# Kernel tuning notes

Hardware: AMD Instinct MI355X
Metric: run time of the kernel (lower is better)

The kernel has to match this reference:

```python
import jax, jax.numpy as jnp
import numpy as np

B, S, D, H, NS = 4, 4096, 1024, 16, 128
DA, DF = 512, 4096
DK, DV = DA // H, D // H  # 32, 64
TEMP = 1.0
EPS = 1e-6


def setup_inputs() -> dict:
    key = jax.random.key(0)
    ks = jax.random.split(key, 8)
    r = lambda k, shp: jax.random.normal(k, shp, jnp.float32) * 0.02
    return dict(
        x=jax.random.normal(ks[0], (B, S, D), jnp.float32),
        mask=jnp.ones((B, S), jnp.float32),
        residual_scale=jnp.ones((1,), jnp.float32),
        w_q=r(ks[1], (D, DA)), b_q=jnp.zeros((DA,), jnp.float32),
        w_kv=r(ks[2], (D, DA + D)), b_kv=jnp.zeros((DA + D,), jnp.float32),
        w_s=r(ks[3], (D, H * NS)), b_s=jnp.zeros((H * NS,), jnp.float32),
        w_cat=r(ks[4], (D, D)), b_cat=jnp.zeros((D,), jnp.float32),
        norm1_w=jnp.ones((D,), jnp.float32), norm2_w=jnp.ones((D,), jnp.float32),
        w1=r(ks[5], (D, DF)), b1=jnp.zeros((DF,), jnp.float32),
        w2=r(ks[6], (DF, D)), b2=jnp.zeros((D,), jnp.float32),
    )


def _rms(x, w):
    return x * jax.lax.rsqrt(jnp.mean(x * x, axis=-1, keepdims=True) + EPS) * w


def _forward(x, mask, residual_scale, w_q, b_q, w_kv, b_kv, w_s, b_s,
             w_cat, b_cat, norm1_w, norm2_w, w1, b1, w2, b2):
    neg = jnp.finfo(jnp.float32).min
    xn = _rms(x, norm1_w)
    q = (xn @ w_q + b_q).reshape(B, S, H, DK).transpose(0, 2, 1, 3)        # [B,H,S,DK]
    kv = (xn @ w_kv + b_kv).reshape(B, S, H, DK + DV).transpose(0, 2, 1, 3)  # [B,H,S,DK+DV]
    k_raw, v_raw = kv[..., :DK], kv[..., DK:]

    # DSZRC sampler: per-head soft routing of S tokens -> NS sampled KV rows
    logits = (x @ w_s + b_s).reshape(B, S, H, NS).transpose(0, 2, 3, 1)    # [B,H,NS,S]
    logits = jnp.where(mask[:, None, None, :] > 0, logits, neg)
    probs = jax.nn.softmax(logits / TEMP, axis=-1)
    kv_s = jnp.einsum('bhms,bhsd->bhmd', probs, kv)                        # [B,H,NS,DK+DV]
    k_s, v_s = kv_s[..., :DK], kv_s[..., DK:]

    # branch 1: dense SDPA over sampled KV
    scale = 1.0 / np.sqrt(DK).astype(np.float32)
    att = jax.nn.softmax(jnp.einsum('bhqd,bhkd->bhqk', q, k_s) * scale, axis=-1)
    out1 = jnp.einsum('bhqk,bhkd->bhqd', att, v_s)                         # [B,H,S,DV]

    # branch 2: fp16 sliding-window flash attn, left window = NS (keys i-NS..i)
    f16 = lambda t: t.astype(jnp.float16).astype(jnp.float32)
    qh, kh, vh = f16(q), f16(k_raw), f16(v_raw)
    bs = NS
    nb = S // bs
    qb = qh.reshape(B, H, nb, bs, DK)
    kb = kh.reshape(B, H, nb, bs, DK)
    vb = vh.reshape(B, H, nb, bs, DV)
    shift = lambda t: jnp.concatenate([jnp.zeros_like(t[:, :, :1]), t[:, :, :-1]], axis=2)
    kctx = jnp.concatenate([shift(kb), kb], axis=3)                        # [B,H,nb,2bs,DK]
    vctx = jnp.concatenate([shift(vb), vb], axis=3)
    sc = jnp.einsum('bhnad,bhnkd->bhnak', qb, kctx) * scale                # [B,H,nb,bs,2bs]
    a = jnp.arange(bs)[:, None]
    bcol = jnp.arange(2 * bs)[None, :]
    band = (bcol >= a) & (bcol <= a + NS)                                  # 0 <= q-k <= NS
    tpos = jnp.arange(nb)[:, None, None]
    valid = band[None] & ((tpos > 0) | (bcol >= bs)[None])                 # no keys before pos 0
    p = jax.nn.softmax(jnp.where(valid[None, None], sc, neg), axis=-1)
    out2 = f16(jnp.einsum('bhnak,bhnkd->bhnad', p, vctx)).reshape(B, H, S, DV)

    x_att = (out1 + out2).transpose(0, 2, 1, 3).reshape(B, S, D)
    x = x + (x_att @ w_cat + b_cat) * residual_scale
    h = _rms(x, norm2_w)
    x = x + (jax.nn.gelu(h @ w1 + b1, approximate=False) @ w2 + b2) * residual_scale
    return x


def reference(x, mask, residual_scale, w_q, b_q, w_kv, b_kv, w_s, b_s,
              w_cat, b_cat, norm1_w, norm2_w, w1, b1, w2, b2):
    return _forward(x, mask, residual_scale, w_q, b_q, w_kv, b_kv, w_s, b_s,
                    w_cat, b_cat, norm1_w, norm2_w, w1, b1, w2, b2)
```

## Files before the change

kernel.cpp:

```cpp
#include <hip/hip_runtime.h>
#include <cstdint>
#include <cmath>

#define DEV __device__ __forceinline__

using f16 = _Float16;
typedef f16  f16x4 __attribute__((ext_vector_type(4)));
typedef f16  f16x8 __attribute__((ext_vector_type(8)));
typedef float f32x4 __attribute__((ext_vector_type(4)));

constexpr int Bq = 4, Sq = 4096, Hq = 16;
constexpr int Tq = Bq * Sq;

DEV void gload_lds16(const void* g, void* l) {
  __builtin_amdgcn_global_load_lds(
      (const __attribute__((address_space(1))) void*)g,
      (__attribute__((address_space(3))) void*)l, 16, 0, 0);
}

DEV void stage_swz(const char* gbase, long gstride, char* lds, int nbytes,
                   int rowlog, int swzmask) {
  int tid = threadIdx.x;
  for (int b0 = 0; b0 < nbytes; b0 += 4096) {
    int P = b0 + tid * 16;
    int L = P ^ (((P >> rowlog) & swzmask) << 4);
    long row  = L >> rowlog;
    int  colb = L & ((1 << rowlog) - 1);
    gload_lds16(gbase + row * gstride + colb, lds + b0 + (tid & ~63) * 16);
  }
}

DEV void stage_swz512(const char* gbase, long gstride, char* lds, int nbytes,
                      int rowlog, int swzmask) {
  int tid = threadIdx.x;
  for (int b0 = 0; b0 < nbytes; b0 += 8192) {
    int P = b0 + tid * 16;
    int L = P ^ (((P >> rowlog) & swzmask) << 4);
    long row  = L >> rowlog;
    int  colb = L & ((1 << rowlog) - 1);
    gload_lds16(gbase + row * gstride + colb, lds + b0 + (tid & ~63) * 16);
  }
}

DEV void pipe_barrier() {
  __builtin_amdgcn_sched_barrier(0);
  __builtin_amdgcn_s_barrier();
  asm volatile("" ::: "memory");
  __builtin_amdgcn_sched_barrier(0);
}

DEV float wave16_max(float v) {
#pragma unroll
  for (int d = 1; d < 16; d <<= 1) v = fmaxf(v, __shfl_xor(v, d, 64));
  return v;
}
DEV float wave16_sum(float v) {
#pragma unroll
  for (int d = 1; d < 16; d <<= 1) v += __shfl_xor(v, d, 64);
  return v;
}

__global__ __launch_bounds__(256) void wcast_k(const float* __restrict__ W,
                                               f16* __restrict__ Wt, int K, int N) {
  int n0 = blockIdx.x * 32, k0 = blockIdx.y * 32;
  __shared__ float tile[32][33];
  int tid = threadIdx.x, r = tid >> 5, c = tid & 31;
#pragma unroll
  for (int i = 0; i < 4; ++i)
    tile[r + i * 8][c] = W[(size_t)(k0 + r + i * 8) * N + n0 + c];
  __syncthreads();
#pragma unroll
  for (int i = 0; i < 4; ++i) {
    int rr = r + i * 8;
    Wt[(size_t)(n0 + rr) * K + k0 + c] = (f16)tile[c][rr];
  }
}

__global__ void bias_concat_k(const float* __restrict__ bq, const float* __restrict__ bkv,
                              float* __restrict__ out) {
  int i = blockIdx.x * 256 + threadIdx.x;
  out[i] = (i < 512) ? bq[i] : bkv[i - 512];
}

__global__ __launch_bounds__(256) void rmsnorm_k(const float* __restrict__ x,
                                                 const float* __restrict__ w,
                                                 f16* __restrict__ xn) {
  int row = blockIdx.x, tid = threadIdx.x;
  float4 v = ((const float4*)(x + (size_t)row * 1024))[tid];
  float ss = v.x * v.x + v.y * v.y + v.z * v.z + v.w * v.w;
#pragma unroll
  for (int d = 1; d < 64; d <<= 1) ss += __shfl_xor(ss, d, 64);
  __shared__ float red[4];
  if ((tid & 63) == 0) red[tid >> 6] = ss;
  __syncthreads();
  float tot = red[0] + red[1] + red[2] + red[3];
  float r = rsqrtf(tot * (1.0f / 1024.0f) + 1e-6f);
  float4 wv = ((const float4*)w)[tid];
  f16x4 o;
  o[0] = (f16)(v.x * r * wv.x); o[1] = (f16)(v.y * r * wv.y);
  o[2] = (f16)(v.z * r * wv.z); o[3] = (f16)(v.w * r * wv.w);
  *(f16x4*)(xn + (size_t)row * 1024 + tid * 4) = o;
}

template <int MODE>
__global__ __launch_bounds__(256) void gemm_k(const f16* __restrict__ A, const f16* __restrict__ Bt,
                                              const float* __restrict__ bias,
                                              float* __restrict__ outF,
                                              const float* __restrict__ resid,
                                              const float* __restrict__ rsp,
                                              int M, int N, int K, int lda, int ldb) {
  __shared__ alignas(16) char smA[2][16384];
  __shared__ alignas(16) char smB[2][16384];
  int nwgx = gridDim.x, nbc = gridDim.y;
  int bidl = blockIdx.y * nwgx + blockIdx.x;
  int cpx = (nwgx * nbc) >> 3;
  int xcd = bidl & 7, pos = bidl >> 3;
  int rpm = cpx / nbc;
  int nbi = pos / rpm, mbi = pos % rpm;
  int mb = xcd * rpm + mbi;
  long n0 = (long)nbi * 128;
  int tid = threadIdx.x, lane = tid & 63, wv = tid >> 6, wr = wv >> 1, wc = wv & 1;
  long m0 = (long)mb * 128;
  f32x4 acc[4][4] = {};
  const char* Ab = (MODE == 7) ? nullptr : (const char*)(A + m0 * lda);
  const char* Bb = (const char*)(Bt + n0 * ldb);

  auto stageAB = [&](int buf, int k0) {
    stage_swz(Bb + (long)k0 * 2, (long)ldb * 2, smB[buf], 16384, 7, 7);
    if (MODE == 7) {
      const char* Ab7 = (const char*)(A + (((m0 >> 12) * 16 + (k0 >> 6)) * 4096 + (m0 & 4095)) * 64);
      stage_swz(Ab7, 128, smA[buf], 16384, 7, 7);
    } else {
      stage_swz(Ab + (long)k0 * 2, (long)lda * 2, smA[buf], 16384, 7, 7);
    }
  };
  auto doCompute = [&](const char* cA, const char* cB) {
#pragma unroll
    for (int kk = 0; kk < 2; ++kk) {
      int kbyte = kk * 64 + (lane >> 4) * 16;
      f16x8 aF[4], bF[4];
#pragma unroll
      for (int m = 0; m < 4; ++m) {
        int L = (wr * 64 + m * 16 + (lane & 15)) * 128 + kbyte;
        aF[m] = *(const f16x8*)(cA + (L ^ (((L >> 7) & 7) << 4)));
      }
#pragma unroll
      for (int n = 0; n < 4; ++n) {
        int L = (wc * 64 + n * 16 + (lane & 15)) * 128 + kbyte;
        bF[n] = *(const f16x8*)(cB + (L ^ (((L >> 7) & 7) << 4)));
      }
#pragma unroll
      for (int m = 0; m < 4; ++m)
#pragma unroll
        for (int n = 0; n < 4; ++n)
          acc[m][n] = __builtin_amdgcn_mfma_f32_16x16x32_f16(aF[m], bF[n], acc[m][n], 0, 0, 0);
    }
  };

  int T = K >> 6;
  stageAB(0, 0);
  stageAB(1, 64);
  asm volatile("s_waitcnt vmcnt(8)" ::: "memory");
  pipe_barrier();
  for (int t = 0; t < T; ++t) {
    doCompute(smA[t & 1], smB[t & 1]);
    pipe_barrier();
    if (t + 2 < T) {
      stageAB(t & 1, (t + 2) << 6);
      asm volatile("s_waitcnt vmcnt(8)" ::: "memory");
    } else {
      asm volatile("s_waitcnt vmcnt(0)" ::: "memory");
    }
    if (t + 1 < T) pipe_barrier();
  }
  float rsv = rsp[0];
#pragma unroll
  for (int m = 0; m < 4; ++m)
#pragma unroll
    for (int n = 0; n < 4; ++n) {
      long gn = n0 + wc * 64 + n * 16 + (lane & 15);
      float bv = bias[gn];
      long rbase = m0 + wr * 64 + m * 16 + (lane >> 4) * 4;
#pragma unroll
      for (int i = 0; i < 4; ++i) {
        long gm = rbase + i;
        float v = acc[m][n][i] + bv;
        long idx = gm * N + gn;
        outF[idx] = resid[idx] + v * rsv;
      }
    }
}

template <int MODE>
__global__ __launch_bounds__(512) void gemm256_k(const f16* __restrict__ A, const f16* __restrict__ Bt,
                                                 const float* __restrict__ bias,
                                                 f16* __restrict__ o1, f16* __restrict__ o2,
                                                 f16* __restrict__ o3,
                                                 const float* __restrict__ resid,
                                                 int M, int N, int K, int lda, int ldb, int pp) {
  __shared__ alignas(16) char smA[2][32768];
  __shared__ alignas(16) char smB[2][32768];
  int nwgx = gridDim.x, nbc = gridDim.y;
  int bidl = blockIdx.y * nwgx + blockIdx.x;
  int cpx = (nwgx * nbc) >> 3;
  int xcd = bidl & 7, pos = bidl >> 3;
  int rpm = cpx / nbc;
  int nbi = pos / rpm, mbi = pos % rpm;
  int mb = xcd * rpm + mbi;
  long n0 = (long)nbi * 256;
  int tid = threadIdx.x, lane = tid & 63, wv = tid >> 6;
  int wr = wv >> 2, wc = wv & 3;
  long m0;
  long t0 = 0;
  int bq = 0;
  if (MODE == 5) {
    bq = mb >> 3; int sb = mb & 7;
    m0 = (long)sb * 256;
    t0 = (long)bq * 4096 + (long)pp * 2048 + m0;
  } else {
    m0 = (long)mb * 256;
  }
  f32x4 acc[8][4] = {};
  const char* Ab = (MODE == 5) ? nullptr : (const char*)(A + m0 * lda);
  const char* Bb = (const char*)(Bt + n0 * ldb);

  auto stageAB = [&](int buf, int k0) {
    stage_swz512(Bb + (long)k0 * 2, (long)ldb * 2, smB[buf], 32768, 7, 7);
    if (MODE == 5) {
      int P = tid * 16;
#pragma unroll
      for (int b0 = 0; b0 < 32768; b0 += 8192) {
        int PP = b0 + P;
        int L = PP ^ (((PP >> 7) & 7) << 4);
        int row = L >> 7, colf = (L & 127) >> 1;
        const float* src = resid + (size_t)(t0 + row) * 1024 + k0 + colf;
        float4 u0 = *(const float4*)src;
        float4 u1 = *(const float4*)(src + 4);
        f16x8 o;
        o[0] = (f16)u0.x; o[1] = (f16)u0.y; o[2] = (f16)u0.z; o[3] = (f16)u0.w;
        o[4] = (f16)u1.x; o[5] = (f16)u1.y; o[6] = (f16)u1.z; o[7] = (f16)u1.w;
        *(f16x8*)(smA[buf] + PP) = o;
      }
    } else {
      stage_swz512(Ab + (long)k0 * 2, (long)lda * 2, smA[buf], 32768, 7, 7);
    }
  };
  auto doCompute = [&](const char* cA, const char* cB) {
#pragma unroll
    for (int kk = 0; kk < 2; ++kk) {
      int kbyte = kk * 64 + (lane >> 4) * 16;
      f16x8 aF[8], bF[4];
#pragma unroll
      for (int m = 0; m < 8; ++m) {
        int L = (wr * 128 + m * 16 + (lane & 15)) * 128 + kbyte;
        aF[m] = *(const f16x8*)(cA + (L ^ (((L >> 7) & 7) << 4)));
      }
#pragma unroll
      for (int n = 0; n < 4; ++n) {
        int L = (wc * 64 + n * 16 + (lane & 15)) * 128 + kbyte;
        bF[n] = *(const f16x8*)(cB + (L ^ (((L >> 7) & 7) << 4)));
      }
#pragma unroll
      for (int m = 0; m < 8; ++m)
#pragma unroll
        for (int n = 0; n < 4; ++n)
          acc[m][n] = __builtin_amdgcn_mfma_f32_16x16x32_f16(aF[m], bF[n], acc[m][n], 0, 0, 0);
    }
  };

  if constexpr (MODE == 5) {
    stageAB(0, 0);
    __syncthreads();
    int cur = 0;
    for (int k0 = 0; k0 < K; k0 += 64) {
      if (k0 + 64 < K) stageAB(cur ^ 1, k0 + 64);
      doCompute(smA[cur], smB[cur]);
      __syncthreads();
      cur ^= 1;
    }
  } else {
    int T = K >> 6;
    stageAB(0, 0);
    stageAB(1, 64);
    asm volatile("s_waitcnt vmcnt(8)" ::: "memory");
    pipe_barrier();
    for (int t = 0; t < T; ++t) {
      doCompute(smA[t & 1], smB[t & 1]);
      pipe_barrier();
      if (t + 2 < T) {
        stageAB(t & 1, (t + 2) << 6);
        asm volatile("s_waitcnt vmcnt(8)" ::: "memory");
      } else {
        asm volatile("s_waitcnt vmcnt(0)" ::: "memory");
      }
      if (t + 1 < T) pipe_barrier();
    }
  }
#pragma unroll
  for (int m = 0; m < 8; ++m)
#pragma unroll
    for (int n = 0; n < 4; ++n) {
      long gn = n0 + wc * 64 + n * 16 + (lane & 15);
      float bv = bias[gn];
      long rbase = m0 + wr * 128 + m * 16 + (lane >> 4) * 4;
      if (MODE == 4) {
        long b = rbase >> 12, s = rbase & 4095;
        if (gn < 512) {
          long h = gn >> 5, dk = gn & 31;
#pragma unroll
          for (int i = 0; i < 4; ++i)
            o1[(((size_t)b * 16 + h) * 4096 + s + i) * 32 + dk] = (f16)(acc[m][n][i] + bv);
        } else {
          long c2 = gn - 512, h = c2 / 96, j = c2 % 96;
          if (j < 32) {
#pragma unroll
            for (int i = 0; i < 4; ++i)
              o2[(((size_t)b * 16 + h) * 4096 + s + i) * 32 + j] = (f16)(acc[m][n][i] + bv);
          } else {
            f16x4 pk;
#pragma unroll
            for (int i = 0; i < 4; ++i) pk[i] = (f16)(acc[m][n][i] + bv);
            *(f16x4*)(o3 + (((size_t)b * 16 + h) * 64 + (j - 32)) * 4096 + s) = pk;
          }
        }
      } else {
#pragma unroll
        for (int i = 0; i < 4; ++i) {
          long gm = rbase + i;
          float v = acc[m][n][i] + bv;
          if (MODE == 3) {
            float u = v * 0.7978845608028654f * (1.f + 0.044715f * v * v);
            float e = __expf(fminf(2.f * u, 80.f));
            o1[gm * N + gn] = (f16)(v * (e / (e + 1.f)));
          } else {
            o1[((size_t)bq * 2048 + gn) * 2048 + gm] = (f16)v;
          }
        }
      }
    }
}

__global__ __launch_bounds__(256) void kvs_k(const f16* __restrict__ lt,
                                             const f16* __restrict__ kh,
                                             const f16* __restrict__ vT,
                                             const float* __restrict__ mask,
                                             float* __restrict__ pacc, int pass) {
  int gx = blockIdx.x, nsb = gx & 3, sc = gx >> 2;
  int h = blockIdx.y, b = blockIdx.z;
  int bh = b * 16 + h;
  __shared__ alignas(16) char smA[4096];
  __shared__ alignas(16) f16 smB[112][88];
  int tid = threadIdx.x, lane = tid & 63, w = tid >> 6;
  int mf = w >> 1, nb0 = (w & 1) * 4, nfr = (w & 1) ? 3 : 4;
  for (int idx = tid; idx < 16 * 64; idx += 256) {
    int r = 96 + (idx >> 6), c2 = idx & 63;
    smB[r][c2] = (r == 96) ? (f16)1.0f : (f16)0.0f;
  }
  f32x4 acc[4] = {};
  const f16* ltb = lt + ((size_t)bh * 128 + nsb * 32) * 2048;
  for (int it = 0; it < 4; ++it) {
    int sl0 = sc * 256 + it * 64;
    int s0g = pass * 2048 + sl0;
    __syncthreads();
    {
      int P = tid * 16;
      int L = P ^ (((P >> 7) & 7) << 4);
      int row = L >> 7, colf = (L & 127) >> 1;
      f16x8 lv = *(const f16x8*)(ltb + (size_t)row * 2048 + sl0 + colf);
      const float* mrow = mask + (size_t)b * 4096 + s0g + colf;
      float4 m0v = *(const float4*)mrow, m1v = *(const float4*)(mrow + 4);
      float mm[8] = {m0v.x, m0v.y, m0v.z, m0v.w, m1v.x, m1v.y, m1v.z, m1v.w};
      f16x8 o;
#pragma unroll
      for (int j = 0; j < 8; ++j)
        o[j] = (f16)((mm[j] > 0.f) ? expf((float)lv[j] - 8.0f) : 0.0f);
      *(f16x8*)(smA + P) = o;
    }
    {
      int sl = tid >> 2, jg = (tid & 3) * 8;
      f16x8 u = *(const f16x8*)(kh + ((size_t)bh * 4096 + s0g + sl) * 32 + jg);
#pragma unroll
      for (int j = 0; j < 8; ++j) smB[jg + j][sl] = u[j];
    }
#pragma unroll
    for (int half = 0; half < 2; ++half) {
      int task = tid + half * 256;
      int dv = task >> 3, sl0v = (task & 7) * 8;
      f16x8 u = *(const f16x8*)(vT + ((size_t)bh * 64 + dv) * 4096 + s0g + sl0v);
      *(f16x8*)(&smB[32 + dv][sl0v]) = u;
    }
    __syncthreads();
#pragma unroll
    for (int kk = 0; kk < 2; ++kk) {
      int kbyte = kk * 64 + (lane >> 4) * 16;
      int L = (mf * 16 + (lane & 15)) * 128 + kbyte;
      f16x8 aF = *(const f16x8*)(smA + (L ^ (((L >> 7) & 7) << 4)));
#pragma unroll
      for (int n = 0; n < 4; ++n)
        if (n < nfr) {
          f16x8 bF = *(const f16x8*)((const char*)smB + ((nb0 + n) * 16 + (lane & 15)) * 176 + kbyte);
          acc[n] = __builtin_amdgcn_mfma_f32_16x16x32_f16(aF, bF, acc[n], 0, 0, 0);
        }
    }
  }
  int slot = pass * 8 + sc;
  float* pb = pacc + (((size_t)bh * 4 + nsb) * 16 + slot) * 3584;
#pragma unroll
  for (int n = 0; n < 4; ++n)
    if (n < nfr) {
      int col = (nb0 + n) * 16 + (lane & 15);
#pragma unroll
      for (int i = 0; i < 4; ++i) {
        int nsrow = mf * 16 + (lane >> 4) * 4 + i;
        pb[(size_t)nsrow * 112 + col] = acc[n][i];
      }
    }
}

__global__ __launch_bounds__(256) void kvs_fin_k(const float* __restrict__ pacc,
                                                 f16* __restrict__ ks, f16* __restrict__ vst) {
  int bh = blockIdx.x, tid = threadIdx.x;
  __shared__ float den[128];
  const float* base = pacc + (size_t)bh * 4 * 16 * 3584;
  if (tid < 128) {
    int nsb = tid >> 5, nsl = tid & 31;
    float d = 0.f;
#pragma unroll
    for (int slot = 0; slot < 16; ++slot)
      d += base[((size_t)nsb * 16 + slot) * 3584 + (size_t)nsl * 112 + 96];
    den[tid] = d;
  }
  __syncthreads();
  for (int e = tid; e < 12288; e += 256) {
    int ns = e / 96, j = e % 96;
    int nsb = ns >> 5, nsl = ns & 31;
    float sv = 0.f;
#pragma unroll
    for (int slot = 0; slot < 16; ++slot)
      sv += base[((size_t)nsb * 16 + slot) * 3584 + (size_t)nsl * 112 + j];
    float v = sv / den[ns];
    if (j < 32) ks[((size_t)bh * 128 + ns) * 32 + j] = (f16)v;
    else        vst[((size_t)bh * 64 + (j - 32)) * 128 + ns] = (f16)v;
  }
}

__global__ __launch_bounds__(256) void att_k(const f16* __restrict__ qh,
                                             const f16* __restrict__ kh,
                                             const f16* __restrict__ vTh,
                                             const f16* __restrict__ ksb,
                                             const f16* __restrict__ vstb,
                                             f16* __restrict__ xatt) {
  int ntj = blockIdx.x, h = blockIdx.y, b = blockIdx.z;
  int nt = ((ntj & 7) << 3) | (ntj >> 3);
  int bh = b * 16 + h, s0 = nt * 64;
  __shared__ alignas(16) char smQ[4096];
  __shared__ alignas(16) char smK[4096];
  __shared__ alignas(16) char smV[8192];
  __shared__ alignas(16) f16 smP[4][16][72];
  int tid = threadIdx.x, lane = tid & 63, w = tid >> 6;
  const float scale = 0.17677669529663687f;
  stage_swz((const char*)(qh + ((size_t)bh * 4096 + s0) * 32), 64, smQ, 4096, 6, 3);

  float mrun[4], lrun[4], m1[4], l1[4];
#pragma unroll
  for (int i = 0; i < 4; ++i) { mrun[i] = -1e30f; lrun[i] = 0.f; m1[i] = -1e30f; l1[i] = 0.f; }
  f32x4 o2[4] = {}, o1[4] = {};

  for (int c = 0; c < 5; ++c) {
    bool win = (c < 3);
    long kb = (long)s0 + (c - 2) * 64;
    if (win && kb < 0) continue;
    __syncthreads();
    if (win) {
      stage_swz((const char*)(kh + ((size_t)bh * 4096 + kb) * 32), 64, smK, 4096, 6, 3);
      stage_swz((const char*)(vTh + (size_t)bh * 64 * 4096 + kb), 8192, smV, 8192, 7, 7);
    } else {
      int sc = c - 3;
      stage_swz((const char*)(ksb + ((size_t)bh * 128 + sc * 64) * 32), 64, smK, 4096, 6, 3);
      stage_swz((const char*)(vstb + (size_t)bh * 64 * 128 + sc * 64), 256, smV, 8192, 7, 7);
    }
    __syncthreads();
    f32x4 s[4] = {};
    {
      int kbyte = (lane >> 4) * 16;
      int Lq = (w * 16 + (lane & 15)) * 64 + kbyte;
      f16x8 aF = *(const f16x8*)(smQ + (Lq ^ (((Lq >> 6) & 3) << 4)));
#pragma unroll
      for (int n = 0; n < 4; ++n) {
        int Lk = (n * 16 + (lane & 15)) * 64 + kbyte;
        f16x8 bF = *(const f16x8*)(smK + (Lk ^ (((Lk >> 6) & 3) << 4)));
        s[n] = __builtin_amdgcn_mfma_f32_16x16x32_f16(aF, bF, s[n], 0, 0, 0);
      }
    }
    float* mr = win ? mrun : m1;
    float* lr = win ? lrun : l1;
    f32x4* oo = win ? o2 : o1;
#pragma unroll
    for (int i = 0; i < 4; ++i) {
      int a2 = w * 16 + (lane >> 4) * 4 + i;
      float nm = mr[i];
#pragma unroll
      for (int n = 0; n < 4; ++n) {
        int kl = n * 16 + (lane & 15);
        bool valid = !win || (c == 1) || (c == 0 ? (kl >= a2) : (kl <= a2));
        float v = valid ? s[n][i] * scale : -1e30f;
        s[n][i] = v; nm = fmaxf(nm, v);
      }
      nm = wave16_max(nm);
      float alpha = expf(mr[i] - nm);
      float sum = 0.f;
#pragma unroll
      for (int n = 0; n < 4; ++n) { float p = expf(s[n][i] - nm); s[n][i] = p; sum += p; }
      sum = wave16_sum(sum);
      lr[i] = lr[i] * alpha + sum;
      mr[i] = nm;
#pragma unroll
      for (int n = 0; n < 4; ++n) oo[n][i] *= alpha;
    }
#pragma unroll
    for (int n = 0; n < 4; ++n)
#pragma unroll
      for (int i = 0; i < 4; ++i)
        smP[w][(lane >> 4) * 4 + i][n * 16 + (lane & 15)] = (f16)s[n][i];
#pragma unroll
    for (int kk = 0; kk < 2; ++kk) {
      int kb2 = kk * 64 + (lane >> 4) * 16;
      f16x8 aP = *(const f16x8*)((const char*)smP[w] + (lane & 15) * 144 + kb2);
#pragma unroll
      for (int n = 0; n < 4; ++n) {
        int dv = n * 16 + (lane & 15);
        int Lv = dv * 128 + kb2;
        f16x8 bV = *(const f16x8*)(smV + (Lv ^ (((Lv >> 7) & 7) << 4)));
        oo[n] = __builtin_amdgcn_mfma_f32_16x16x32_f16(aP, bV, oo[n], 0, 0, 0);
      }
    }
  }
  f16* xb = xatt + ((size_t)bh * 4096 + s0) * 64;
#pragma unroll
  for (int n = 0; n < 4; ++n)
#pragma unroll
    for (int i = 0; i < 4; ++i) {
      int row = w * 16 + (lane >> 4) * 4 + i, dv = n * 16 + (lane & 15);
      xb[(size_t)row * 64 + dv] = (f16)(o2[n][i] / lrun[i] + o1[n][i] / l1[i]);
    }
}

__global__ void sentinel_k(float* out, size_t n, float val) {
  size_t i = (size_t)blockIdx.x * 256 + threadIdx.x;
  size_t stride = (size_t)gridDim.x * 256;
  for (; i < n; i += stride) out[i] = val;
}

constexpr size_t OFF_WQKV = 0;
constexpr size_t OFF_WSC  = OFF_WQKV + 2048ull * 1024 * 2;
constexpr size_t OFF_WCAT = OFF_WSC  + 2048ull * 1024 * 2;
constexpr size_t OFF_W1   = OFF_WCAT + 1024ull * 1024 * 2;
constexpr size_t OFF_W2   = OFF_W1   + 4096ull * 1024 * 2;
constexpr size_t OFF_BQKV = OFF_W2   + 1024ull * 4096 * 2;
constexpr size_t OFF_ZB   = OFF_BQKV + 8192;
constexpr size_t OFF_Q    = OFF_ZB   + 4096;
constexpr size_t OFF_K    = OFF_Q    + (size_t)Tq * 512 * 2;
constexpr size_t OFF_P1   = OFF_K    + (size_t)Tq * 512 * 2;
constexpr size_t OFF_VT   = OFF_P1   + (size_t)Tq * 1024 * 2;
constexpr size_t OFF_KVA  = OFF_VT   + (size_t)Tq * 1024 * 2;
constexpr size_t OFF_KS   = OFF_KVA  + 64ull * 128 * 112 * 4;
constexpr size_t OFF_VST  = OFF_KS   + 64ull * 128 * 32 * 2;
constexpr size_t WS_NEED  = OFF_VST  + 64ull * 64 * 128 * 2;

extern "C" void kernel_launch(void* const* d_in, const int* in_sizes, int n_in,
                              void* d_out, int out_size, void* d_ws, size_t ws_size,
                              hipStream_t stream) {
  float* xo = (float*)d_out;
  if (ws_size < WS_NEED) {
    float val = -(1000.0f + (float)(ws_size / 1000000ull));
    sentinel_k<<<2048, 256, 0, stream>>>(xo, (size_t)out_size, val);
    return;
  }
  const float* x     = (const float*)d_in[0];
  const float* mask  = (const float*)d_in[1];
  const float* rsp   = (const float*)d_in[2];
  const float* w_q   = (const float*)d_in[3];
  const float* b_q   = (const float*)d_in[4];
  const float* w_kv  = (const float*)d_in[5];
  const float* b_kv  = (const float*)d_in[6];
  const float* w_s   = (const float*)d_in[7];
  const float* b_s   = (const float*)d_in[8];
  const float* w_cat = (const float*)d_in[9];
  const float* b_cat = (const float*)d_in[10];
  const float* n1w   = (const float*)d_in[11];
  const float* n2w   = (const float*)d_in[12];
  const float* w1    = (const float*)d_in[13];
  const float* b1    = (const float*)d_in[14];
  const float* w2    = (const float*)d_in[15];
  const float* b2    = (const float*)d_in[16];
  char* ws = (char*)d_ws;

  f16*   wqkv_t = (f16*)(ws + OFF_WQKV);
  f16*   ws_t   = (f16*)(ws + OFF_WSC);
  f16*   wcat_t = (f16*)(ws + OFF_WCAT);
  f16*   w1_t   = (f16*)(ws + OFF_W1);
  f16*   w2_t   = (f16*)(ws + OFF_W2);
  float* bqkv   = (float*)(ws + OFF_BQKV);
  f16*   q_h    = (f16*)(ws + OFF_Q);
  f16*   k_h    = (f16*)(ws + OFF_K);
  f16*   h_h    = (f16*)(ws + OFF_Q);
  f16*   xn_h   = (f16*)(ws + OFF_P1);
  f16*   lt16   = (f16*)(ws + OFF_P1);
  f16*   xatt_h = (f16*)(ws + OFF_P1);
  f16*   g_h    = (f16*)(ws + OFF_P1);
  f16*   vT_h   = (f16*)(ws + OFF_VT);
  f16*   ks_h   = (f16*)(ws + OFF_KS);
  f16*   vst_h  = (f16*)(ws + OFF_VST);

  wcast_k<<<dim3(16, 32),  256, 0, stream>>>(w_q,   wqkv_t,              1024, 512);
  wcast_k<<<dim3(48, 32),  256, 0, stream>>>(w_kv,  wqkv_t + 512 * 1024, 1024, 1536);
  wcast_k<<<dim3(64, 32),  256, 0, stream>>>(w_s,   ws_t,                1024, 2048);
  wcast_k<<<dim3(32, 32),  256, 0, stream>>>(w_cat, wcat_t,              1024, 1024);
  wcast_k<<<dim3(128, 32), 256, 0, stream>>>(w1,    w1_t,                1024, 4096);
  wcast_k<<<dim3(32, 128), 256, 0, stream>>>(w2,    w2_t,                4096, 1024);
  bias_concat_k<<<8, 256, 0, stream>>>(b_q, b_kv, bqkv);

  rmsnorm_k<<<Tq, 256, 0, stream>>>(x, n1w, xn_h);
  gemm256_k<4><<<dim3(64, 8), 512, 0, stream>>>(xn_h, wqkv_t, bqkv, q_h, k_h, vT_h,
                                                nullptr, Tq, 2048, 1024, 1024, 1024, 0);
  for (int p = 0; p < 2; ++p) {
    gemm256_k<5><<<dim3(32, 8), 512, 0, stream>>>(nullptr, ws_t, b_s, lt16, nullptr, nullptr,
                                                  x, 8192, 2048, 1024, 0, 1024, p);
    kvs_k<<<dim3(32, 16, 4), 256, 0, stream>>>(lt16, k_h, vT_h, mask, xo, p);
  }
  kvs_fin_k<<<64, 256, 0, stream>>>(xo, ks_h, vst_h);
  att_k<<<dim3(64, 16, 4), 256, 0, stream>>>(q_h, k_h, vT_h, ks_h, vst_h, xatt_h);
  gemm_k<7><<<dim3(128, 8), 256, 0, stream>>>(xatt_h, wcat_t, b_cat, xo,
                                              x, rsp, Tq, 1024, 1024, 0, 1024);
  rmsnorm_k<<<Tq, 256, 0, stream>>>(xo, n2w, h_h);
  for (int mc = 0; mc < 2; ++mc) {
    const f16* hA = h_h + (size_t)mc * 8192 * 1024;
    float* xoc = xo + (size_t)mc * 8192 * 1024;
    gemm256_k<3><<<dim3(32, 16), 512, 0, stream>>>(hA, w1_t, b1, g_h, nullptr, nullptr,
                                                   nullptr, 8192, 4096, 1024, 1024, 1024, 0);
    gemm_k<2><<<dim3(64, 8), 256, 0, stream>>>(g_h, w2_t, b2, xoc,
                                               xoc, rsp, 8192, 1024, 4096, 4096, 4096);
  }
}
```

Before: 949.8 us.

## Interleave split LDS staging with per-column MFMA phases in GEMM main loops

Restructures the GEMM main loops so global-to-LDS staging of the next A/B tiles is split into halves and issued between four MFMA phases, one per B column block. A fragments for both k-steps are loaded once per tile. Each MFMA phase is wrapped in raised wave priority and sched barriers. Launch bounds now request two blocks per CU. The goal is to hide memory latency behind compute and raise occupancy, at the cost of more register pressure and finer-grained waitcnt logic that could stall or spill.

```diff
diff --git a/kernel.cpp b/kernel.cpp
--- a/kernel.cpp
+++ b/kernel.cpp
@@ -103,12 +103,12 @@
 }
 
 template <int MODE>
-__global__ __launch_bounds__(256) void gemm_k(const f16* __restrict__ A, const f16* __restrict__ Bt,
-                                              const float* __restrict__ bias,
-                                              float* __restrict__ outF,
-                                              const float* __restrict__ resid,
-                                              const float* __restrict__ rsp,
-                                              int M, int N, int K, int lda, int ldb) {
+__global__ __launch_bounds__(256, 2) void gemm_k(const f16* __restrict__ A, const f16* __restrict__ Bt,
+                                                 const float* __restrict__ bias,
+                                                 float* __restrict__ outF,
+                                                 const float* __restrict__ resid,
+                                                 const float* __restrict__ rsp,
+                                                 int M, int N, int K, int lda, int ldb) {
   __shared__ alignas(16) char smA[2][16384];
   __shared__ alignas(16) char smB[2][16384];
   int nwgx = gridDim.x, nbc = gridDim.y;
@@ -125,53 +125,112 @@
   const char* Ab = (MODE == 7) ? nullptr : (const char*)(A + m0 * lda);
   const char* Bb = (const char*)(Bt + n0 * ldb);
 
-  auto stageAB = [&](int buf, int k0) {
-    stage_swz(Bb + (long)k0 * 2, (long)ldb * 2, smB[buf], 16384, 7, 7);
+  auto gstage = [&](const char* gbase, long gstride, char* lds, int half) {
+#pragma unroll
+    for (int c = 0; c < 2; ++c) {
+      int b0 = half * 8192 + c * 4096;
+      int P = b0 + tid * 16;
+      int L = P ^ (((P >> 7) & 7) << 4);
+      long row = L >> 7; int colb = L & 127;
+      gload_lds16(gbase + row * gstride + colb, lds + b0 + (tid & ~63) * 16);
+    }
+  };
+  auto stageAh = [&](int buf, int k0, int half) {
     if (MODE == 7) {
       const char* Ab7 = (const char*)(A + (((m0 >> 12) * 16 + (k0 >> 6)) * 4096 + (m0 & 4095)) * 64);
-      stage_swz(Ab7, 128, smA[buf], 16384, 7, 7);
+      gstage(Ab7, 128, smA[buf], half);
     } else {
-      stage_swz(Ab + (long)k0 * 2, (long)lda * 2, smA[buf], 16384, 7, 7);
+      gstage(Ab + (long)k0 * 2, (long)lda * 2, smA[buf], half);
     }
   };
-  auto doCompute = [&](const char* cA, const char* cB) {
+  auto stageBh = [&](int buf, int k0, int half) {
+    gstage(Bb + (long)k0 * 2, (long)ldb * 2, smB[buf], half);
+  };
+
+  int T = K >> 6;
+  int kbyte = (lane >> 4) * 16;
+  stageAh(0, 0, 0); stageAh(0, 0, 1);
+  stageBh(0, 0, 0); stageBh(0, 0, 1);
+  if (T > 1) { stageAh(1, 64, 0); stageAh(1, 64, 1);
+               asm volatile("s_waitcnt vmcnt(4)" ::: "memory"); }
+  else       { asm volatile("s_waitcnt vmcnt(0)" ::: "memory"); }
+  pipe_barrier();
+
+  for (int t = 0; t < T; ++t) {
+    const char* cA = smA[t & 1];
+    const char* cB = smB[t & 1];
+    int nb_ = (t & 1) ^ 1;
+    f16x8 aF[2][4], bN[2];
+    if (t + 1 < T) stageBh(nb_, (t + 1) << 6, 0);
+#pragma unroll
+    for (int kk = 0; kk < 2; ++kk)
+#pragma unroll
+      for (int m = 0; m < 4; ++m) {
+        int L = (wr * 64 + m * 16 + (lane & 15)) * 128 + kk * 64 + kbyte;
+        aF[kk][m] = *(const f16x8*)(cA + (L ^ (((L >> 7) & 7) << 4)));
+      }
 #pragma unroll
     for (int kk = 0; kk < 2; ++kk) {
-      int kbyte = kk * 64 + (lane >> 4) * 16;
-      f16x8 aF[4], bF[4];
-#pragma unroll
-      for (int m = 0; m < 4; ++m) {
-        int L = (wr * 64 + m * 16 + (lane & 15)) * 128 + kbyte;
-        aF[m] = *(const f16x8*)(cA + (L ^ (((L >> 7) & 7) << 4)));
-      }
-#pragma unroll
-      for (int n = 0; n < 4; ++n) {
-        int L = (wc * 64 + n * 16 + (lane & 15)) * 128 + kbyte;
-        bF[n] = *(const f16x8*)(cB + (L ^ (((L >> 7) & 7) << 4)));
-      }
-#pragma unroll
-      for (int m = 0; m < 4; ++m)
-#pragma unroll
-        for (int n = 0; n < 4; ++n)
-          acc[m][n] = __builtin_amdgcn_mfma_f32_16x16x32_f16(aF[m], bF[n], acc[m][n], 0, 0, 0);
-    }
-  };
-
-  int T = K >> 6;
-  stageAB(0, 0);
-  stageAB(1, 64);
-  asm volatile("s_waitcnt vmcnt(8)" ::: "memory");
-  pipe_barrier();
-  for (int t = 0; t < T; ++t) {
-    doCompute(smA[t & 1], smB[t & 1]);
+      int L = (wc * 64 + (lane & 15)) * 128 + kk * 64 + kbyte;
+      bN[kk] = *(const f16x8*)(cB + (L ^ (((L >> 7) & 7) << 4)));
+    }
+    asm volatile("s_waitcnt lgkmcnt(0)" ::: "memory");
+    __builtin_amdgcn_sched_barrier(0);
+    __builtin_amdgcn_s_setprio(1);
+#pragma unroll
+    for (int m = 0; m < 4; ++m)
+#pragma unroll
+      for (int kk = 0; kk < 2; ++kk)
+        acc[m][0] = __builtin_amdgcn_mfma_f32_16x16x32_f16(aF[kk][m], bN[kk], acc[m][0], 0, 0, 0);
+    __builtin_amdgcn_s_setprio(0);
     pipe_barrier();
-    if (t + 2 < T) {
-      stageAB(t & 1, (t + 2) << 6);
-      asm volatile("s_waitcnt vmcnt(8)" ::: "memory");
-    } else {
-      asm volatile("s_waitcnt vmcnt(0)" ::: "memory");
-    }
-    if (t + 1 < T) pipe_barrier();
+    if (t + 1 < T) stageBh(nb_, (t + 1) << 6, 1);
+    if (t + 2 < T) stageAh(t & 1, (t + 2) << 6, 0);
+#pragma unroll
+    for (int kk = 0; kk < 2; ++kk) {
+      int L = (wc * 64 + 16 + (lane & 15)) * 128 + kk * 64 + kbyte;
+      bN[kk] = *(const f16x8*)(cB + (L ^ (((L >> 7) & 7) << 4)));
+    }
+    asm volatile("s_waitcnt lgkmcnt(0)" ::: "memory");
+    __builtin_amdgcn_sched_barrier(0);
+    __builtin_amdgcn_s_setprio(1);
+#pragma unroll
+    for (int m = 0; m < 4; ++m)
+#pragma unroll
+      for (int kk = 0; kk < 2; ++kk)
+        acc[m][1] = __builtin_amdgcn_mfma_f32_16x16x32_f16(aF[kk][m], bN[kk], acc[m][1], 0, 0, 0);
+    __builtin_amdgcn_s_setprio(0);
+    if (t + 2 < T) stageAh(t & 1, (t + 2) << 6, 1);
+#pragma unroll
+    for (int kk = 0; kk < 2; ++kk) {
+      int L = (wc * 64 + 32 + (lane & 15)) * 128 + kk * 64 + kbyte;
+      bN[kk] = *(const f16x8*)(cB + (L ^ (((L >> 7) & 7) << 4)));
+    }
+    asm volatile("s_waitcnt lgkmcnt(0)" ::: "memory");
+    __builtin_amdgcn_sched_barrier(0);
+    __builtin_amdgcn_s_setprio(1);
+#pragma unroll
+    for (int m = 0; m < 4; ++m)
+#pragma unroll
+      for (int kk = 0; kk < 2; ++kk)
+        acc[m][2] = __builtin_amdgcn_mfma_f32_16x16x32_f16(aF[kk][m], bN[kk], acc[m][2], 0, 0, 0);
+    __builtin_amdgcn_s_setprio(0);
+#pragma unroll
+    for (int kk = 0; kk < 2; ++kk) {
+      int L = (wc * 64 + 48 + (lane & 15)) * 128 + kk * 64 + kbyte;
+      bN[kk] = *(const f16x8*)(cB + (L ^ (((L >> 7) & 7) << 4)));
+    }
+    if (t + 2 < T) asm volatile("s_waitcnt vmcnt(4) lgkmcnt(0)" ::: "memory");
+    else           asm volatile("s_waitcnt vmcnt(0) lgkmcnt(0)" ::: "memory");
+    __builtin_amdgcn_sched_barrier(0);
+    __builtin_amdgcn_s_setprio(1);
+#pragma unroll
+    for (int m = 0; m < 4; ++m)
+#pragma unroll
+      for (int kk = 0; kk < 2; ++kk)
+        acc[m][3] = __builtin_amdgcn_mfma_f32_16x16x32_f16(aF[kk][m], bN[kk], acc[m][3], 0, 0, 0);
+    __builtin_amdgcn_s_setprio(0);
+    pipe_barrier();
   }
   float rsv = rsp[0];
 #pragma unroll
@@ -192,12 +251,12 @@
 }
 
 template <int MODE>
-__global__ __launch_bounds__(512) void gemm256_k(const f16* __restrict__ A, const f16* __restrict__ Bt,
-                                                 const float* __restrict__ bias,
-                                                 f16* __restrict__ o1, f16* __restrict__ o2,
-                                                 f16* __restrict__ o3,
-                                                 const float* __restrict__ resid,
-                                                 int M, int N, int K, int lda, int ldb, int pp) {
+__global__ __launch_bounds__(512, 2) void gemm256_k(const f16* __restrict__ A, const f16* __restrict__ Bt,
+                                                    const float* __restrict__ bias,
+                                                    f16* __restrict__ o1, f16* __restrict__ o2,
+                                                    f16* __restrict__ o3,
+                                                    const float* __restrict__ resid,
+                                                    int M, int N, int K, int lda, int ldb, int pp) {
   __shared__ alignas(16) char smA[2][32768];
   __shared__ alignas(16) char smB[2][32768];
   int nwgx = gridDim.x, nbc = gridDim.y;
@@ -224,9 +283,27 @@
   const char* Ab = (MODE == 5) ? nullptr : (const char*)(A + m0 * lda);
   const char* Bb = (const char*)(Bt + n0 * ldb);
 
-  auto stageAB = [&](int buf, int k0) {
-    stage_swz512(Bb + (long)k0 * 2, (long)ldb * 2, smB[buf], 32768, 7, 7);
-    if (MODE == 5) {
+  auto gstage = [&](const char* gbase, long gstride, char* lds, int half) {
+#pragma unroll
+    for (int c = 0; c < 2; ++c) {
+      int b0 = half * 16384 + c * 8192;
+      int P = b0 + tid * 16;
+      int L = P ^ (((P >> 7) & 7) << 4);
+      long row = L >> 7; int colb = L & 127;
+      gload_lds16(gbase + row * gstride + colb, lds + b0 + (tid & ~63) * 16);
+    }
+  };
+  auto stageAh = [&](int buf, int k0, int half) {
+    gstage(Ab + (long)k0 * 2, (long)lda * 2, smA[buf], half);
+  };
+  auto stageBh = [&](int buf, int k0, int half) {
+    gstage(Bb + (long)k0 * 2, (long)ldb * 2, smB[buf], half);
+  };
+  int kbyte = (lane >> 4) * 16;
+
+  if constexpr (MODE == 5) {
+    auto stageAB5 = [&](int buf, int k0) {
+      stage_swz512(Bb + (long)k0 * 2, (long)ldb * 2, smB[buf], 32768, 7, 7);
       int P = tid * 16;
 #pragma unroll
       for (int b0 = 0; b0 < 32768; b0 += 8192) {
@@ -241,59 +318,118 @@
         o[4] = (f16)u1.x; o[5] = (f16)u1.y; o[6] = (f16)u1.z; o[7] = (f16)u1.w;
         *(f16x8*)(smA[buf] + PP) = o;
       }
-    } else {
-      stage_swz512(Ab + (long)k0 * 2, (long)lda * 2, smA[buf], 32768, 7, 7);
-    }
-  };
-  auto doCompute = [&](const char* cA, const char* cB) {
-#pragma unroll
-    for (int kk = 0; kk < 2; ++kk) {
-      int kbyte = kk * 64 + (lane >> 4) * 16;
-      f16x8 aF[8], bF[4];
-#pragma unroll
-      for (int m = 0; m < 8; ++m) {
-        int L = (wr * 128 + m * 16 + (lane & 15)) * 128 + kbyte;
-        aF[m] = *(const f16x8*)(cA + (L ^ (((L >> 7) & 7) << 4)));
-      }
-#pragma unroll
-      for (int n = 0; n < 4; ++n) {
-        int L = (wc * 64 + n * 16 + (lane & 15)) * 128 + kbyte;
-        bF[n] = *(const f16x8*)(cB + (L ^ (((L >> 7) & 7) << 4)));
-      }
-#pragma unroll
-      for (int m = 0; m < 8; ++m)
-#pragma unroll
-        for (int n = 0; n < 4; ++n)
-          acc[m][n] = __builtin_amdgcn_mfma_f32_16x16x32_f16(aF[m], bF[n], acc[m][n], 0, 0, 0);
-    }
-  };
-
-  if constexpr (MODE == 5) {
-    stageAB(0, 0);
+    };
+    stageAB5(0, 0);
     __syncthreads();
     int cur = 0;
     for (int k0 = 0; k0 < K; k0 += 64) {
-      if (k0 + 64 < K) stageAB(cur ^ 1, k0 + 64);
-      doCompute(smA[cur], smB[cur]);
+      if (k0 + 64 < K) stageAB5(cur ^ 1, k0 + 64);
+#pragma unroll
+      for (int kk = 0; kk < 2; ++kk) {
+        int kb2 = kk * 64 + kbyte;
+        f16x8 aF[8], bF[4];
+#pragma unroll
+        for (int m = 0; m < 8; ++m) {
+          int L = (wr * 128 + m * 16 + (lane & 15)) * 128 + kb2;
+          aF[m] = *(const f16x8*)(smA[cur] + (L ^ (((L >> 7) & 7) << 4)));
+        }
+#pragma unroll
+        for (int n = 0; n < 4; ++n) {
+          int L = (wc * 64 + n * 16 + (lane & 15)) * 128 + kb2;
+          bF[n] = *(const f16x8*)(smB[cur] + (L ^ (((L >> 7) & 7) << 4)));
+        }
+#pragma unroll
+        for (int m = 0; m < 8; ++m)
+#pragma unroll
+          for (int n = 0; n < 4; ++n)
+            acc[m][n] = __builtin_amdgcn_mfma_f32_16x16x32_f16(aF[m], bF[n], acc[m][n], 0, 0, 0);
+      }
       __syncthreads();
       cur ^= 1;
     }
   } else {
     int T = K >> 6;
-    stageAB(0, 0);
-    stageAB(1, 64);
-    asm volatile("s_waitcnt vmcnt(8)" ::: "memory");
+    stageAh(0, 0, 0); stageAh(0, 0, 1);
+    stageBh(0, 0, 0); stageBh(0, 0, 1);
+    if (T > 1) { stageAh(1, 64, 0); stageAh(1, 64, 1);
+                 asm volatile("s_waitcnt vmcnt(4)" ::: "memory"); }
+    else       { asm volatile("s_waitcnt vmcnt(0)" ::: "memory"); }
     pipe_barrier();
     for (int t = 0; t < T; ++t) {
-      doCompute(smA[t & 1], smB[t & 1]);
+      const char* cA = smA[t & 1];
+      const char* cB = smB[t & 1];
+      int nb_ = (t & 1) ^ 1;
+      f16x8 aF[2][8], bN[2];
+      if (t + 1 < T) stageBh(nb_, (t + 1) << 6, 0);
+#pragma unroll
+      for (int kk = 0; kk < 2; ++kk)
+#pragma unroll
+        for (int m = 0; m < 8; ++m) {
+          int L = (wr * 128 + m * 16 + (lane & 15)) * 128 + kk * 64 + kbyte;
+          aF[kk][m] = *(const f16x8*)(cA + (L ^ (((L >> 7) & 7) << 4)));
+        }
+#pragma unroll
+      for (int kk = 0; kk < 2; ++kk) {
+        int L = (wc * 64 + (lane & 15)) * 128 + kk * 64 + kbyte;
+        bN[kk] = *(const f16x8*)(cB + (L ^ (((L >> 7) & 7) << 4)));
+      }
+      asm volatile("s_waitcnt lgkmcnt(0)" ::: "memory");
+      __builtin_amdgcn_sched_barrier(0);
+      __builtin_amdgcn_s_setprio(1);
+#pragma unroll
+      for (int m = 0; m < 8; ++m)
+#pragma unroll
+        for (int kk = 0; kk < 2; ++kk)
+          acc[m][0] = __builtin_amdgcn_mfma_f32_16x16x32_f16(aF[kk][m], bN[kk], acc[m][0], 0, 0, 0);
+      __builtin_amdgcn_s_setprio(0);
       pipe_barrier();
-      if (t + 2 < T) {
-        stageAB(t & 1, (t + 2) << 6);
-        asm volatile("s_waitcnt vmcnt(8)" ::: "memory");
-      } else {
-        asm volatile("s_waitcnt vmcnt(0)" ::: "memory");
-      }
-      if (t + 1 < T) pipe_barrier();
+      if (t + 1 < T) stageBh(nb_, (t + 1) << 6, 1);
+      if (t + 2 < T) stageAh(t & 1, (t + 2) << 6, 0);
+#pragma unroll
+      for (int kk = 0; kk < 2; ++kk) {
+        int L = (wc * 64 + 16 + (lane & 15)) * 128 + kk * 64 + kbyte;
+        bN[kk] = *(const f16x8*)(cB + (L ^ (((L >> 7) & 7) << 4)));
+      }
+      asm volatile("s_waitcnt lgkmcnt(0)" ::: "memory");
+      __builtin_amdgcn_sched_barrier(0);
+      __builtin_amdgcn_s_setprio(1);
+#pragma unroll
+      for (int m = 0; m < 8; ++m)
+#pragma unroll
+        for (int kk = 0; kk < 2; ++kk)
+          acc[m][1] = __builtin_amdgcn_mfma_f32_16x16x32_f16(aF[kk][m], bN[kk], acc[m][1], 0, 0, 0);
+      __builtin_amdgcn_s_setprio(0);
+      if (t + 2 < T) stageAh(t & 1, (t + 2) << 6, 1);
+#pragma unroll
+      for (int kk = 0; kk < 2; ++kk) {
+        int L = (wc * 64 + 32 + (lane & 15)) * 128 + kk * 64 + kbyte;
+        bN[kk] = *(const f16x8*)(cB + (L ^ (((L >> 7) & 7) << 4)));
+      }
+      asm volatile("s_waitcnt lgkmcnt(0)" ::: "memory");
+      __builtin_amdgcn_sched_barrier(0);
+      __builtin_amdgcn_s_setprio(1);
+#pragma unroll
+      for (int m = 0; m < 8; ++m)
+#pragma unroll
+        for (int kk = 0; kk < 2; ++kk)
+          acc[m][2] = __builtin_amdgcn_mfma_f32_16x16x32_f16(aF[kk][m], bN[kk], acc[m][2], 0, 0, 0);
+      __builtin_amdgcn_s_setprio(0);
+#pragma unroll
+      for (int kk = 0; kk < 2; ++kk) {
+        int L = (wc * 64 + 48 + (lane & 15)) * 128 + kk * 64 + kbyte;
+        bN[kk] = *(const f16x8*)(cB + (L ^ (((L >> 7) & 7) << 4)));
+      }
+      if (t + 2 < T) asm volatile("s_waitcnt vmcnt(4) lgkmcnt(0)" ::: "memory");
+      else           asm volatile("s_waitcnt vmcnt(0) lgkmcnt(0)" ::: "memory");
+      __builtin_amdgcn_sched_barrier(0);
+      __builtin_amdgcn_s_setprio(1);
+#pragma unroll
+      for (int m = 0; m < 8; ++m)
+#pragma unroll
+        for (int kk = 0; kk < 2; ++kk)
+          acc[m][3] = __builtin_amdgcn_mfma_f32_16x16x32_f16(aF[kk][m], bN[kk], acc[m][3], 0, 0, 0);
+      __builtin_amdgcn_s_setprio(0);
+      pipe_barrier();
     }
   }
 #pragma unroll
```

New measurement: 1.001 ms. +5.4%, slower.
